# Performance work log

Measured on AMD Instinct MI355X. Metric: run time of the kernel, lower is better.

Reference implementation:

```python
import jax, jax.numpy as jnp
import numpy as np

B, N, E, FIN, H, D = 256, 1024, 8192, 8, 4, 5
HD = H * D            # GATv2: 4 heads * 5 dim, concat -> 20
OBS = N               # flattened obs length
AOUT = 64             # action_space_output_dim (aggregator output)
HID = 256             # hidden_size
NOUT = 64             # num_outputs (logits)
NEG = 0.2             # GATv2 leaky_relu negative slope
EPS = 1e-5            # batchnorm eps


def setup_inputs() -> dict:
    key = jax.random.key(0)
    ks = jax.random.split(key, 16)
    def lin(k, i, o):
        return (jax.random.normal(k, (i, o), jnp.float32) / np.sqrt(i)).astype(jnp.float32)
    return {
        "x": jax.random.normal(ks[0], (B, N, FIN), jnp.float32),
        "obs": jax.random.normal(ks[1], (B, OBS), jnp.float32),
        "edge_index": jax.random.randint(ks[2], (2, E), 0, N),
        # GATv2 layer 0 (in=FIN) and layer 1 (in=HD)
        "Wl0": lin(ks[3], FIN, HD), "Wr0": lin(ks[4], FIN, HD),
        "att0": (jax.random.normal(ks[5], (H, D), jnp.float32) * 0.1), "b0": jnp.zeros((HD,), jnp.float32),
        "Wl1": lin(ks[6], HD, HD), "Wr1": lin(ks[7], HD, HD),
        "att1": (jax.random.normal(ks[8], (H, D), jnp.float32) * 0.1), "b1": jnp.zeros((HD,), jnp.float32),
        # BatchNorm params per layer (over feature dim)
        "g0": jnp.ones((HD,), jnp.float32), "be0": jnp.zeros((HD,), jnp.float32),
        "g1": jnp.ones((HD,), jnp.float32), "be1": jnp.zeros((HD,), jnp.float32),
        # aggregator linear (mean pool -> action-space dim)
        "Wagg": lin(ks[9], HD, AOUT), "bagg": jnp.zeros((AOUT,), jnp.float32),
        # logits MLP: cat(agg, obs) -> HID -> HID//2 -> NOUT (tanh activations)
        "W1": lin(ks[10], AOUT + OBS, HID), "bh1": jnp.zeros((HID,), jnp.float32),
        "W2": lin(ks[11], HID, HID // 2), "bh2": jnp.zeros((HID // 2,), jnp.float32),
        "Wout": lin(ks[12], HID // 2, NOUT), "bout": jnp.zeros((NOUT,), jnp.float32),
    }


def _gatv2_single(x, src, dst, Wl, Wr, att, bias):
    # x: [N, Fin]; src/dst: [Es] (with self loops)
    xl = (x @ Wl).reshape(N, H, D)
    xr = (x @ Wr).reshape(N, H, D)
    m = jax.nn.leaky_relu(xl[src] + xr[dst], NEG)        # [Es, H, D]
    e = jnp.einsum('ehd,hd->eh', m, att)                 # [Es, H]
    emax = jax.ops.segment_max(e, dst, num_segments=N)   # every node has a self loop
    p = jnp.exp(e - emax[dst])
    s = jax.ops.segment_sum(p, dst, num_segments=N)
    alpha = p / s[dst]                                   # softmax over incoming edges
    out = jax.ops.segment_sum(alpha[:, :, None] * xl[src], dst, num_segments=N)
    return out.reshape(N, HD) + bias


def _bn(x, g, b):
    # training-mode batchnorm over all (batch, node) positions, per feature
    mu = x.mean(axis=(0, 1))
    var = x.var(axis=(0, 1))
    return (x - mu) * jax.lax.rsqrt(var + EPS) * g + b


def reference(x, obs, edge_index, Wl0, Wr0, att0, b0, Wl1, Wr1, att1, b1,
              g0, be0, g1, be1, Wagg, bagg, W1, bh1, W2, bh2, Wout, bout):
    loops = jnp.arange(N)
    src = jnp.concatenate([edge_index[0], loops])
    dst = jnp.concatenate([edge_index[1], loops])
    layer = lambda xb, Wl, Wr, att, bias: jax.vmap(
        lambda xn: _gatv2_single(xn, src, dst, Wl, Wr, att, bias))(xb)
    h = layer(x, Wl0, Wr0, att0, b0)       # [B, N, HD]
    h = _bn(h, g0, be0)
    h = layer(h, Wl1, Wr1, att1, b1)
    h = _bn(h, g1, be1)
    agg = h.mean(axis=1) @ Wagg + bagg     # mean graph pooling -> [B, AOUT]
    f = jnp.concatenate([agg, obs], axis=1)
    f = jnp.tanh(f @ W1 + bh1)
    f = jnp.tanh(f @ W2 + bh2)
    return f @ Wout + bout                 # logits [B, NOUT]
```

## Files before the change

### kernel.cpp

```cpp
#include <hip/hip_runtime.h>
#include <hip/hip_bf16.h>
#include <math.h>

typedef unsigned short u16;
typedef __attribute__((ext_vector_type(8))) short short8;
typedef __attribute__((ext_vector_type(4))) float floatx4;

constexpr int kN   = 1024;
constexpr int kB   = 256;
constexpr int kE   = 8192;
constexpr int kHD  = 20;
constexpr float kEps = 1e-5f;

static __device__ __forceinline__ float u16_bf16_to_f32(u16 v) {
  return __uint_as_float(((unsigned)v) << 16);
}
static __device__ __forceinline__ void unpack2(unsigned u, float& a, float& b) {
  a = __uint_as_float(u << 16);
  b = __uint_as_float(u & 0xffff0000u);
}
static __device__ __forceinline__ u16 f2bf(float f) {
  __hip_bfloat16 h = __float2bfloat16(f);
  return *reinterpret_cast<u16*>(&h);
}
static __device__ __forceinline__ unsigned pack_bf16(float a, float b) {
  return (unsigned)f2bf(a) | ((unsigned)f2bf(b) << 16);
}

__global__ __launch_bounds__(64) void detect_kernel(const unsigned* __restrict__ x,
                                                    int* __restrict__ flag) {
  unsigned w = x[threadIdx.x];
  unsigned e = (w >> 7) & 0xFFu;
  bool plaus = (e >= 114u && e <= 136u);
  unsigned long long b = __ballot(plaus);
  if (threadIdx.x == 0) *flag = (__popcll(b) >= 32) ? 1 : 0;
}

struct SmallConv {
  const void* src[17];
  float* dst[17];
  int n[17];
};

__global__ __launch_bounds__(256) void small_conv_kernel(SmallConv a, const int* __restrict__ flag) {
  int t = blockIdx.x;
  int n = a.n[t];
  float* d = a.dst[t];
  if (*flag) {
    const u16* s = (const u16*)a.src[t];
    for (int i = threadIdx.x; i < n; i += 256) d[i] = u16_bf16_to_f32(s[i]);
  } else {
    const float* s = (const float*)a.src[t];
    for (int i = threadIdx.x; i < n; i += 256) d[i] = s[i];
  }
}

__global__ __launch_bounds__(256) void convert_x_kernel(const void* __restrict__ src,
                                                        float* __restrict__ x_f,
                                                        const int* __restrict__ flag) {
  int rid = blockIdx.x * 256 + threadIdx.x;
  int b = rid >> 10, n = rid & 1023;
  float v[8];
  if (*flag) {
    uint4 r = *((const uint4*)((const u16*)src + (size_t)rid * 8));
    unpack2(r.x, v[0], v[1]); unpack2(r.y, v[2], v[3]);
    unpack2(r.z, v[4], v[5]); unpack2(r.w, v[6], v[7]);
  } else {
    const float4* s = (const float4*)((const float*)src + (size_t)rid * 8);
    float4 r0 = s[0], r1 = s[1];
    v[0] = r0.x; v[1] = r0.y; v[2] = r0.z; v[3] = r0.w;
    v[4] = r1.x; v[5] = r1.y; v[6] = r1.z; v[7] = r1.w;
  }
  float* d = x_f + ((size_t)n * kB + b) * 8;
  ((float4*)d)[0] = make_float4(v[0], v[1], v[2], v[3]);
  ((float4*)d)[1] = make_float4(v[4], v[5], v[6], v[7]);
}

static __device__ __forceinline__ void repack_one(const void* src, u16* dst, int c, int N, int srcbf) {
  int n = c % N;
  int t2 = c / N;
  int q = t2 & 3, kb = t2 >> 2;
  int k0 = kb * 32 + q * 8;
  u16 w[8];
  if (srcbf) {
    const u16* s = (const u16*)src;
#pragma unroll
    for (int j = 0; j < 8; j++) w[j] = s[(size_t)(k0 + j) * N + n];
  } else {
    const float* s = (const float*)src;
#pragma unroll
    for (int j = 0; j < 8; j++) w[j] = f2bf(s[(size_t)(k0 + j) * N + n]);
  }
  uint4 out;
  out.x = (unsigned)w[0] | ((unsigned)w[1] << 16);
  out.y = (unsigned)w[2] | ((unsigned)w[3] << 16);
  out.z = (unsigned)w[4] | ((unsigned)w[5] << 16);
  out.w = (unsigned)w[6] | ((unsigned)w[7] << 16);
  *((uint4*)(dst + (size_t)c * 8)) = out;
}

__global__ __launch_bounds__(256) void repack_kernel(const void* __restrict__ W1,
                                                     const void* __restrict__ W2,
                                                     const void* __restrict__ Wout,
                                                     u16* __restrict__ W1p,
                                                     u16* __restrict__ W2p,
                                                     u16* __restrict__ Woutp,
                                                     const int* __restrict__ flag) {
  int c = blockIdx.x * 256 + threadIdx.x;
  int srcbf = *flag;
  if (c < 34816) repack_one(W1, W1p, c, 256, srcbf);
  else if (c < 34816 + 4096) repack_one(W2, W2p, c - 34816, 128, srcbf);
  else if (c < 34816 + 4096 + 1024) repack_one(Wout, Woutp, c - 34816 - 4096, 64, srcbf);
}

__global__ __launch_bounds__(1024) void build_csr_kernel(const int* __restrict__ ei,
                                                         int* __restrict__ csr_off,
                                                         int* __restrict__ csr_src) {
  __shared__ int cnt[kN];
  __shared__ int tmp[kN];
  __shared__ int cur[kN];
  int t = threadIdx.x;
  cnt[t] = 0;
  __syncthreads();
  for (int e = t; e < kE; e += 1024) atomicAdd(&cnt[ei[kE + e]], 1);
  __syncthreads();
  int deg = cnt[t] + 1;
  tmp[t] = deg;
  __syncthreads();
  for (int o = 1; o < kN; o <<= 1) {
    int add = (t >= o) ? tmp[t - o] : 0;
    __syncthreads();
    tmp[t] += add;
    __syncthreads();
  }
  int excl = tmp[t] - deg;
  csr_off[t] = excl;
  cur[t] = excl;
  if (t == kN - 1) csr_off[kN] = tmp[t];
  __syncthreads();
  for (int e = t; e < kE; e += 1024) {
    int s = ei[e], d2 = ei[kE + e];
    int pos = atomicAdd(&cur[d2], 1);
    csr_src[pos] = s;
  }
  int pos = atomicAdd(&cur[t], 1);
  csr_src[pos] = t;
}

__global__ __launch_bounds__(256) void lin0_kernel(const float* __restrict__ x,
                                                   const float* __restrict__ Wl,
                                                   const float* __restrict__ Wr,
                                                   u16* __restrict__ xlb,
                                                   u16* __restrict__ xrb) {
  __shared__ float wl[8 * kHD], wr[8 * kHD];
  int t = threadIdx.x;
  if (t < 8 * kHD) { wl[t] = Wl[t]; wr[t] = Wr[t]; }
  __syncthreads();
  int n = blockIdx.x, b = t;
  const float4* xp = (const float4*)(x + ((size_t)n * kB + b) * 8);
  float xi[8];
  {
    float4 v0 = xp[0], v1 = xp[1];
    xi[0] = v0.x; xi[1] = v0.y; xi[2] = v0.z; xi[3] = v0.w;
    xi[4] = v1.x; xi[5] = v1.y; xi[6] = v1.z; xi[7] = v1.w;
  }
  float ol[kHD], orr[kHD];
#pragma unroll
  for (int f = 0; f < kHD; f++) {
    float al = 0.f, ar = 0.f;
#pragma unroll
    for (int i = 0; i < 8; i++) {
      al = fmaf(xi[i], wl[i * kHD + f], al);
      ar = fmaf(xi[i], wr[i * kHD + f], ar);
    }
    ol[f] = al; orr[f] = ar;
  }
  uint2* pl = (uint2*)(xlb + ((size_t)n * kB + b) * kHD);
  uint2* pr = (uint2*)(xrb + ((size_t)n * kB + b) * kHD);
#pragma unroll
  for (int k = 0; k < 5; k++) {
    pl[k] = make_uint2(pack_bf16(ol[4 * k], ol[4 * k + 1]), pack_bf16(ol[4 * k + 2], ol[4 * k + 3]));
    pr[k] = make_uint2(pack_bf16(orr[4 * k], orr[4 * k + 1]), pack_bf16(orr[4 * k + 2], orr[4 * k + 3]));
  }
}

__global__ __launch_bounds__(256) void lin1_kernel(const u16* __restrict__ hb,
                                                   const float* __restrict__ Wlp,
                                                   const float* __restrict__ Wrp,
                                                   const float* __restrict__ blp,
                                                   const float* __restrict__ brp,
                                                   u16* __restrict__ xlb,
                                                   u16* __restrict__ xrb) {
  __shared__ float wl[kHD * kHD], wr[kHD * kHD], sbl[kHD], sbr[kHD];
  int t = threadIdx.x;
  for (int idx = t; idx < kHD * kHD; idx += 256) { wl[idx] = Wlp[idx]; wr[idx] = Wrp[idx]; }
  if (t < kHD) { sbl[t] = blp[t]; sbr[t] = brp[t]; }
  __syncthreads();
  int n = blockIdx.x, b = t;
  float hv[kHD];
  {
    const uint2* p = (const uint2*)(hb + ((size_t)n * kB + b) * kHD);
#pragma unroll
    for (int k = 0; k < 5; k++) {
      uint2 v = p[k];
      unpack2(v.x, hv[4 * k], hv[4 * k + 1]);
      unpack2(v.y, hv[4 * k + 2], hv[4 * k + 3]);
    }
  }
  float ol[kHD], orr[kHD];
#pragma unroll
  for (int j = 0; j < kHD; j++) {
    float al = sbl[j], ar = sbr[j];
#pragma unroll
    for (int f = 0; f < kHD; f++) {
      al = fmaf(hv[f], wl[f * kHD + j], al);
      ar = fmaf(hv[f], wr[f * kHD + j], ar);
    }
    ol[j] = al; orr[j] = ar;
  }
  uint2* pl = (uint2*)(xlb + ((size_t)n * kB + b) * kHD);
  uint2* pr = (uint2*)(xrb + ((size_t)n * kB + b) * kHD);
#pragma unroll
  for (int k = 0; k < 5; k++) {
    pl[k] = make_uint2(pack_bf16(ol[4 * k], ol[4 * k + 1]), pack_bf16(ol[4 * k + 2], ol[4 * k + 3]));
    pr[k] = make_uint2(pack_bf16(orr[4 * k], orr[4 * k + 1]), pack_bf16(orr[4 * k + 2], orr[4 * k + 3]));
  }
}

__global__ __launch_bounds__(128) void attn_kernel(const u16* __restrict__ xlb,
                                                   const u16* __restrict__ xrb,
                                                   const int* __restrict__ csr_off,
                                                   const int* __restrict__ csr_src,
                                                   const float* __restrict__ att,
                                                   const float* __restrict__ bias,
                                                   u16* __restrict__ hout,
                                                   float* __restrict__ sums) {
  __shared__ float satt[kHD], sbias[kHD];
  __shared__ float red[2][2 * kHD];
  int t = threadIdx.x;
  if (t < kHD) { satt[t] = att[t]; sbias[t] = bias[t]; }
  __syncthreads();
  int n = blockIdx.x >> 1;
  int b = ((blockIdx.x & 1) << 7) | t;

  float xrv[kHD];
  {
    const uint2* p = (const uint2*)(xrb + ((size_t)n * kB + b) * kHD);
#pragma unroll
    for (int k = 0; k < 5; k++) {
      uint2 v = p[k];
      unpack2(v.x, xrv[4 * k], xrv[4 * k + 1]);
      unpack2(v.y, xrv[4 * k + 2], xrv[4 * k + 3]);
    }
  }
  float s[4] = {0.f, 0.f, 0.f, 0.f};
  float acc[kHD];
#pragma unroll
  for (int f = 0; f < kHD; f++) acc[f] = 0.f;

  int beg = csr_off[n], end = csr_off[n + 1];
  uint2 r[5];
  {
    const uint2* p = (const uint2*)(xlb + ((size_t)csr_src[beg] * kB + b) * kHD);
#pragma unroll
    for (int k = 0; k < 5; k++) r[k] = p[k];
  }
  for (int idx = beg; idx < end; idx++) {
    float xs[kHD];
#pragma unroll
    for (int k = 0; k < 5; k++) {
      unpack2(r[k].x, xs[4 * k], xs[4 * k + 1]);
      unpack2(r[k].y, xs[4 * k + 2], xs[4 * k + 3]);
    }
    if (idx + 1 < end) {
      const uint2* p = (const uint2*)(xlb + ((size_t)csr_src[idx + 1] * kB + b) * kHD);
#pragma unroll
      for (int k = 0; k < 5; k++) r[k] = p[k];
    }
#pragma unroll
    for (int hh = 0; hh < 4; hh++) {
      float e = 0.f;
#pragma unroll
      for (int d = 0; d < 5; d++) {
        int f = hh * 5 + d;
        float v = xs[f] + xrv[f];
        v = fmaxf(v, 0.2f * v);
        e = fmaf(v, satt[f], e);
      }
      float p = __expf(e);
      s[hh] += p;
#pragma unroll
      for (int d = 0; d < 5; d++) {
        int f = hh * 5 + d;
        acc[f] = fmaf(p, xs[f], acc[f]);
      }
    }
  }
  float hv[kHD];
#pragma unroll
  for (int hh = 0; hh < 4; hh++) {
    float inv = 1.f / s[hh];
#pragma unroll
    for (int d = 0; d < 5; d++) {
      int f = hh * 5 + d;
      hv[f] = fmaf(acc[f], inv, sbias[f]);
    }
  }
  {
    uint2* ph = (uint2*)(hout + ((size_t)n * kB + b) * kHD);
#pragma unroll
    for (int k = 0; k < 5; k++)
      ph[k] = make_uint2(pack_bf16(hv[4 * k], hv[4 * k + 1]), pack_bf16(hv[4 * k + 2], hv[4 * k + 3]));
  }
  int lane = t & 63, wv = t >> 6;
#pragma unroll
  for (int f = 0; f < kHD; f++) {
    float a = hv[f], q = hv[f] * hv[f];
    for (int o = 32; o > 0; o >>= 1) { a += __shfl_down(a, o); q += __shfl_down(q, o); }
    if (lane == 0) { red[wv][f] = a; red[wv][kHD + f] = q; }
  }
  __syncthreads();
  if (t < 2 * kHD) atomicAdd(&sums[(blockIdx.x & 7) * 2 * kHD + t], red[0][t] + red[1][t]);
}

__global__ __launch_bounds__(256) void fold_kernel(const float* __restrict__ sums,
                                                   const float* __restrict__ g,
                                                   const float* __restrict__ be,
                                                   const float* __restrict__ Wl1,
                                                   const float* __restrict__ Wr1,
                                                   float* __restrict__ Wlp, float* __restrict__ Wrp,
                                                   float* __restrict__ blp, float* __restrict__ brp) {
  __shared__ float a[kHD], c[kHD];
  __shared__ float tot[2 * kHD];
  int t = threadIdx.x;
  if (t < 2 * kHD) {
    float v = 0.f;
    for (int k = 0; k < 8; k++) v += sums[k * 2 * kHD + t];
    tot[t] = v;
  }
  __syncthreads();
  if (t < kHD) {
    const float inv = 1.0f / (float)(kN * kB);
    float mu = tot[t] * inv;
    float var = tot[kHD + t] * inv - mu * mu;
    float av = g[t] * rsqrtf(var + kEps);
    a[t] = av;
    c[t] = be[t] - mu * av;
  }
  __syncthreads();
  for (int idx = t; idx < kHD * kHD; idx += 256) {
    int f = idx / kHD;
    Wlp[idx] = a[f] * Wl1[idx];
    Wrp[idx] = a[f] * Wr1[idx];
  }
  if (t < kHD) {
    float sl = 0.f, sr = 0.f;
    for (int f = 0; f < kHD; f++) {
      sl += c[f] * Wl1[f * kHD + t];
      sr += c[f] * Wr1[f * kHD + t];
    }
    blp[t] = sl;
    brp[t] = sr;
  }
}

__global__ __launch_bounds__(256) void pool_fin_kernel(const u16* __restrict__ hb,
                                                       const float* __restrict__ sums,
                                                       const float* __restrict__ g1,
                                                       const float* __restrict__ be1,
                                                       const float* __restrict__ Wagg,
                                                       const float* __restrict__ bagg,
                                                       const void* __restrict__ obsraw,
                                                       const int* __restrict__ flag,
                                                       u16* __restrict__ finb) {
  int b = blockIdx.x, t = threadIdx.x;
  float acc[kHD];
#pragma unroll
  for (int f = 0; f < kHD; f++) acc[f] = 0.f;
  for (int n = t; n < kN; n += 256) {
    const uint2* p = (const uint2*)(hb + ((size_t)n * kB + b) * kHD);
#pragma unroll
    for (int k = 0; k < 5; k++) {
      uint2 v = p[k];
      float a0, a1, a2, a3;
      unpack2(v.x, a0, a1); unpack2(v.y, a2, a3);
      acc[4 * k] += a0; acc[4 * k + 1] += a1; acc[4 * k + 2] += a2; acc[4 * k + 3] += a3;
    }
  }
  __shared__ float red[4][kHD];
// ... 16 lines not shown
    float var = tot[kHD + t] * inv - mu * mu;
    float a1 = g1[t] * rsqrtf(var + kEps);
    float c1 = be1[t] - mu * a1;
    float pool = (red[0][t] + red[1][t] + red[2][t] + red[3][t]) * (1.0f / kN);
    pv[t] = pool * a1 + c1;
  }
  __syncthreads();
  if (t < 64) {
    float agg = bagg[t];
#pragma unroll
    for (int f = 0; f < kHD; f++) agg = fmaf(pv[f], Wagg[f * 64 + t], agg);
    finb[(size_t)b * 1088 + t] = f2bf(agg);
  }
  if (t < 128) {
    uint4* dst = (uint4*)(finb + (size_t)b * 1088 + 64 + t * 8);
    if (*flag) {
      *dst = *((const uint4*)((const u16*)obsraw + (size_t)b * 1024 + t * 8));
    } else {
      const float4* s = (const float4*)((const float*)obsraw + (size_t)b * 1024 + t * 8);
      float4 r0 = s[0], r1 = s[1];
      uint4 o;
      o.x = pack_bf16(r0.x, r0.y); o.y = pack_bf16(r0.z, r0.w);
      o.z = pack_bf16(r1.x, r1.y); o.w = pack_bf16(r1.z, r1.w);
      *dst = o;
    }
  }
}

__global__ __launch_bounds__(256) void mlp1_kernel(const u16* __restrict__ finb,
                                                   const u16* __restrict__ W1p,
                                                   const float* __restrict__ bh1,
                                                   u16* __restrict__ h1b) {
  int tid = threadIdx.x;
  int wave = tid >> 6, lane = tid & 63;
  int tile = blockIdx.x * 4 + wave;
  int m0 = (tile >> 4) << 4, n0 = (tile & 15) << 4;
  int lo = lane & 15, quad = lane >> 4;
  floatx4 acc = {0.f, 0.f, 0.f, 0.f};
  const u16* ap = finb + (size_t)(m0 + lo) * 1088 + quad * 8;
  const u16* bp = W1p + ((size_t)quad * 256 + n0 + lo) * 8;
  for (int kb = 0; kb < 34; kb++) {
    short8 a = *(const short8*)ap; ap += 32;
    short8 bfr = *(const short8*)bp; bp += 4 * 256 * 8;
    acc = __builtin_amdgcn_mfma_f32_16x16x32_bf16(a, bfr, acc, 0, 0, 0);
  }
  float bias = bh1[n0 + lo];
  u16* op = h1b + (size_t)(m0 + quad * 4) * 256 + n0 + lo;
#pragma unroll
  for (int r = 0; r < 4; r++) op[r * 256] = f2bf(tanhf(acc[r] + bias));
}

__global__ __launch_bounds__(256) void mlp23_kernel(const u16* __restrict__ h1b,
                                                    const u16* __restrict__ W2p,
                                                    const u16* __restrict__ Woutp,
                                                    const float* __restrict__ bh2,
                                                    const float* __restrict__ bout,
                                                    const int* __restrict__ flag,
                                                    void* __restrict__ outv) {
  __shared__ __align__(16) u16 h2s[16][128];
  int tid = threadIdx.x;
  int wave = tid >> 6, lane = tid & 63;
  int lo = lane & 15, quad = lane >> 4;
  int m0 = blockIdx.x * 16;
#pragma unroll
  for (int i = 0; i < 2; i++) {
    int n0 = (wave * 2 + i) * 16;
    floatx4 acc = {0.f, 0.f, 0.f, 0.f};
    const u16* ap = h1b + (size_t)(m0 + lo) * 256 + quad * 8;
    const u16* bp = W2p + ((size_t)quad * 128 + n0 + lo) * 8;
    for (int kb = 0; kb < 8; kb++) {
      short8 a = *(const short8*)ap; ap += 32;
      short8 bfr = *(const short8*)bp; bp += 4 * 128 * 8;
      acc = __builtin_amdgcn_mfma_f32_16x16x32_bf16(a, bfr, acc, 0, 0, 0);
    }
    float bias = bh2[n0 + lo];
#pragma unroll
    for (int r = 0; r < 4; r++) h2s[quad * 4 + r][n0 + lo] = f2bf(tanhf(acc[r] + bias));
  }
  __syncthreads();
  {
    int n0 = wave * 16;
    floatx4 acc = {0.f, 0.f, 0.f, 0.f};
    const u16* bp = Woutp + ((size_t)quad * 64 + n0 + lo) * 8;
    for (int kb = 0; kb < 4; kb++) {
      short8 a = *(const short8*)(&h2s[lo][kb * 32 + quad * 8]);
      short8 bfr = *(const short8*)bp; bp += 4 * 64 * 8;
      acc = __builtin_amdgcn_mfma_f32_16x16x32_bf16(a, bfr, acc, 0, 0, 0);
    }
    float bias = bout[n0 + lo];
    if (*flag) {
      __hip_bfloat16* o = (__hip_bfloat16*)outv;
#pragma unroll
      for (int r = 0; r < 4; r++)
        o[(size_t)(m0 + quad * 4 + r) * 64 + n0 + lo] = __float2bfloat16(acc[r] + bias);
    } else {
      float* o = (float*)outv;
#pragma unroll
      for (int r = 0; r < 4; r++)
        o[(size_t)(m0 + quad * 4 + r) * 64 + n0 + lo] = acc[r] + bias;
    }
  }
}

extern "C" void kernel_launch(void* const* d_in, const int* in_sizes, int n_in,
                              void* d_out, int out_size, void* d_ws, size_t ws_size,
                              hipStream_t stream) {
  const int* ei = (const int*)d_in[2];
  char* ws = (char*)d_ws;

  float* sums0   = (float*)(ws + 0);
  float* sums1   = (float*)(ws + 1280);
  int*   flag    = (int*)(ws + 2560);
  int*   csr_off = (int*)(ws + 2816);
  int*   csr_src = (int*)(ws + 7168);
  float* Wlp     = (float*)(ws + 44288);
  float* Wrp     = (float*)(ws + 45888);
  float* blp     = (float*)(ws + 47488);
  float* brp     = (float*)(ws + 47568);
  float* convf   = (float*)(ws + 47872);
  u16*   W1p     = (u16*)(ws + 60416);
  u16*   W2p     = (u16*)(ws + 617472);
  u16*   Woutp   = (u16*)(ws + 683008);
  u16*   finb    = (u16*)(ws + 699392);
  u16*   h1b     = (u16*)(ws + 1256448);
  float* x_f     = (float*)(ws + 1387520);
  u16*   xlb     = (u16*)(ws + 9776128);
  u16*   xrb     = (u16*)(ws + 20261888);
  u16*   hb      = (u16*)(ws + 30747648);

  const int s_din[17] = {3, 4, 5, 6, 7, 8, 9, 10, 11, 12, 13, 14, 15, 16, 18, 20, 22};
  const int s_n[17]   = {160, 160, 20, 20, 400, 400, 20, 20, 20, 20, 20, 20, 1280, 64, 256, 128, 64};
  SmallConv sc;
  float* fptr[17];
  {
    size_t co = 0;
    for (int i = 0; i < 17; i++) {
      sc.src[i] = d_in[s_din[i]];
      sc.dst[i] = convf + co;
      sc.n[i] = s_n[i];
      fptr[i] = convf + co;
      co += (size_t)s_n[i];
    }
  }
  float* Wl0_f = fptr[0],  *Wr0_f = fptr[1],  *att0_f = fptr[2], *b0_f = fptr[3];
  float* Wl1_f = fptr[4],  *Wr1_f = fptr[5],  *att1_f = fptr[6], *b1_f = fptr[7];
  float* g0_f = fptr[8],   *be0_f = fptr[9],  *g1_f = fptr[10],  *be1_f = fptr[11];
  float* Wagg_f = fptr[12], *bagg_f = fptr[13], *bh1_f = fptr[14], *bh2_f = fptr[15];
  float* bout_f = fptr[16];

  hipMemsetAsync(ws, 0, 2560, stream);
  detect_kernel<<<1, 64, 0, stream>>>((const unsigned*)d_in[0], flag);
  small_conv_kernel<<<17, 256, 0, stream>>>(sc, flag);
  convert_x_kernel<<<1024, 256, 0, stream>>>(d_in[0], x_f, flag);
  repack_kernel<<<156, 256, 0, stream>>>(d_in[17], d_in[19], d_in[21], W1p, W2p, Woutp, flag);
  build_csr_kernel<<<1, 1024, 0, stream>>>(ei, csr_off, csr_src);

  lin0_kernel<<<kN, 256, 0, stream>>>(x_f, Wl0_f, Wr0_f, xlb, xrb);
  attn_kernel<<<2 * kN, 128, 0, stream>>>(xlb, xrb, csr_off, csr_src, att0_f, b0_f, hb, sums0);
  fold_kernel<<<1, 256, 0, stream>>>(sums0, g0_f, be0_f, Wl1_f, Wr1_f, Wlp, Wrp, blp, brp);
  lin1_kernel<<<kN, 256, 0, stream>>>(hb, Wlp, Wrp, blp, brp, xlb, xrb);
  attn_kernel<<<2 * kN, 128, 0, stream>>>(xlb, xrb, csr_off, csr_src, att1_f, b1_f, hb, sums1);
  pool_fin_kernel<<<kB, 256, 0, stream>>>(hb, sums1, g1_f, be1_f, Wagg_f, bagg_f,
                                          d_in[1], flag, finb);
  mlp1_kernel<<<64, 256, 0, stream>>>(finb, W1p, bh1_f, h1b);
  mlp23_kernel<<<16, 256, 0, stream>>>(h1b, W2p, Woutp, bh2_f, bout_f, flag, d_out);
}
```

Baseline: 235.8 us.

## Fuse prep kernels, compute xr inside attention, fold BN in-kernel, merge MLP

Merges detect, small-conversion, x-conversion, weight repack and CSR build into one multi-role prep kernel, and replaces the memset. The attention kernels now compute the right-side projection xr per destination node themselves instead of reading a stored xr buffer, which removes one large write and read per layer. The BatchNorm fold moves into lin1 and attn1. The three MLP kernels become a single kernel that keeps intermediates in shared memory. This cuts launch count and global traffic, but adds redundant per-block fold and projection compute, and leaves the MLP running on only 16 blocks.

After: 239.8 us. Within noise of the previous version (+1.7%).

```diff
diff --git a/kernel.cpp b/kernel.cpp
--- a/kernel.cpp
+++ b/kernel.cpp
@@ -27,13 +27,17 @@
   return (unsigned)f2bf(a) | ((unsigned)f2bf(b) << 16);
 }
 
-__global__ __launch_bounds__(64) void detect_kernel(const unsigned* __restrict__ x,
-                                                    int* __restrict__ flag) {
-  unsigned w = x[threadIdx.x];
-  unsigned e = (w >> 7) & 0xFFu;
-  bool plaus = (e >= 114u && e <= 136u);
-  unsigned long long b = __ballot(plaus);
-  if (threadIdx.x == 0) *flag = (__popcll(b) >= 32) ? 1 : 0;
+static __device__ __forceinline__ int detect_flag(const unsigned* __restrict__ x) {
+  __shared__ int sflag;
+  int t = threadIdx.x;
+  if (t < 64) {
+    unsigned w = x[t];
+    unsigned e = (w >> 7) & 0xFFu;
+    unsigned long long bl = __ballot(e >= 114u && e <= 136u);
+    if (t == 0) sflag = (__popcll(bl) >= 32) ? 1 : 0;
+  }
+  __syncthreads();
+  return sflag;
 }
 
 struct SmallConv {
@@ -42,39 +46,16 @@
   int n[17];
 };
 
-__global__ __launch_bounds__(256) void small_conv_kernel(SmallConv a, const int* __restrict__ flag) {
-  int t = blockIdx.x;
-  int n = a.n[t];
-  float* d = a.dst[t];
-  if (*flag) {
-    const u16* s = (const u16*)a.src[t];
-    for (int i = threadIdx.x; i < n; i += 256) d[i] = u16_bf16_to_f32(s[i]);
-  } else {
-    const float* s = (const float*)a.src[t];
-    for (int i = threadIdx.x; i < n; i += 256) d[i] = s[i];
-  }
-}
-
-__global__ __launch_bounds__(256) void convert_x_kernel(const void* __restrict__ src,
-                                                        float* __restrict__ x_f,
-                                                        const int* __restrict__ flag) {
-  int rid = blockIdx.x * 256 + threadIdx.x;
-  int b = rid >> 10, n = rid & 1023;
-  float v[8];
-  if (*flag) {
-    uint4 r = *((const uint4*)((const u16*)src + (size_t)rid * 8));
-    unpack2(r.x, v[0], v[1]); unpack2(r.y, v[2], v[3]);
-    unpack2(r.z, v[4], v[5]); unpack2(r.w, v[6], v[7]);
-  } else {
-    const float4* s = (const float4*)((const float*)src + (size_t)rid * 8);
-    float4 r0 = s[0], r1 = s[1];
-    v[0] = r0.x; v[1] = r0.y; v[2] = r0.z; v[3] = r0.w;
-    v[4] = r1.x; v[5] = r1.y; v[6] = r1.z; v[7] = r1.w;
-  }
-  float* d = x_f + ((size_t)n * kB + b) * 8;
-  ((float4*)d)[0] = make_float4(v[0], v[1], v[2], v[3]);
-  ((float4*)d)[1] = make_float4(v[4], v[5], v[6], v[7]);
-}
+struct PrepArgs {
+  const unsigned* x;
+  const int* ei;
+  const void* W1; const void* W2; const void* Wout;
+  SmallConv sc;
+  float* x_f;
+  u16* W1p; u16* W2p; u16* Woutp;
+  int* csr_off; int* csr_src;
+  float* sums;
+};
 
 static __device__ __forceinline__ void repack_one(const void* src, u16* dst, int c, int N, int srcbf) {
   int n = c % N;
@@ -99,102 +80,146 @@
   *((uint4*)(dst + (size_t)c * 8)) = out;
 }
 
-__global__ __launch_bounds__(256) void repack_kernel(const void* __restrict__ W1,
-                                                     const void* __restrict__ W2,
-                                                     const void* __restrict__ Wout,
-                                                     u16* __restrict__ W1p,
-                                                     u16* __restrict__ W2p,
-                                                     u16* __restrict__ Woutp,
-                                                     const int* __restrict__ flag) {
-  int c = blockIdx.x * 256 + threadIdx.x;
-  int srcbf = *flag;
-  if (c < 34816) repack_one(W1, W1p, c, 256, srcbf);
-  else if (c < 34816 + 4096) repack_one(W2, W2p, c - 34816, 128, srcbf);
-  else if (c < 34816 + 4096 + 1024) repack_one(Wout, Woutp, c - 34816 - 4096, 64, srcbf);
-}
-
-__global__ __launch_bounds__(1024) void build_csr_kernel(const int* __restrict__ ei,
-                                                         int* __restrict__ csr_off,
-                                                         int* __restrict__ csr_src) {
-  __shared__ int cnt[kN];
-  __shared__ int tmp[kN];
-  __shared__ int cur[kN];
+__global__ __launch_bounds__(256) void prep_kernel(PrepArgs pa) {
+  int bid = blockIdx.x;
   int t = threadIdx.x;
-  cnt[t] = 0;
-  __syncthreads();
-  for (int e = t; e < kE; e += 1024) atomicAdd(&cnt[ei[kE + e]], 1);
-  __syncthreads();
-  int deg = cnt[t] + 1;
-  tmp[t] = deg;
-  __syncthreads();
-  for (int o = 1; o < kN; o <<= 1) {
-    int add = (t >= o) ? tmp[t - o] : 0;
+  if (bid == 0) {
+    __shared__ int cnt[kN];
+    __shared__ int cur[kN];
+    __shared__ int wsum[4];
+    for (int i = t; i < kN; i += 256) cnt[i] = 0;
     __syncthreads();
-    tmp[t] += add;
+    for (int e = t; e < kE; e += 256) atomicAdd(&cnt[pa.ei[kE + e]], 1);
     __syncthreads();
-  }
-  int excl = tmp[t] - deg;
-  csr_off[t] = excl;
-  cur[t] = excl;
-  if (t == kN - 1) csr_off[kN] = tmp[t];
-  __syncthreads();
-  for (int e = t; e < kE; e += 1024) {
-    int s = ei[e], d2 = ei[kE + e];
-    int pos = atomicAdd(&cur[d2], 1);
-    csr_src[pos] = s;
-  }
-  int pos = atomicAdd(&cur[t], 1);
-  csr_src[pos] = t;
-}
-
-__global__ __launch_bounds__(256) void lin0_kernel(const float* __restrict__ x,
+    int d[4], pre[4];
+    int s = 0;
+#pragma unroll
+    for (int j = 0; j < 4; j++) { d[j] = cnt[t * 4 + j] + 1; pre[j] = s; s += d[j]; }
+    int lane = t & 63;
+    int v = s;
+    for (int o = 1; o < 64; o <<= 1) { int u = __shfl_up(v, o); if (lane >= o) v += u; }
+    if (lane == 63) wsum[t >> 6] = v;
+    __syncthreads();
+    int wbase = 0;
+    for (int w = 0; w < (t >> 6); w++) wbase += wsum[w];
+    int base = wbase + v - s;
+#pragma unroll
+    for (int j = 0; j < 4; j++) {
+      pa.csr_off[t * 4 + j] = base + pre[j];
+      cur[t * 4 + j] = base + pre[j];
+    }
+    if (t == 255) pa.csr_off[kN] = wbase + v;
+    __syncthreads();
+    for (int e = t; e < kE; e += 256) {
+      int sv = pa.ei[e], dv = pa.ei[kE + e];
+      int pos = atomicAdd(&cur[dv], 1);
+      pa.csr_src[pos] = sv;
+    }
+    for (int i = t; i < kN; i += 256) {
+      int pos = atomicAdd(&cur[i], 1);
+      pa.csr_src[pos] = i;
+    }
+    return;
+  }
+  int flag = detect_flag(pa.x);
+  if (bid == 1) {
+    for (int i = t; i < 640; i += 256) pa.sums[i] = 0.f;
+    for (int k = 0; k < 17; k++) {
+      int n = pa.sc.n[k];
+      float* d = pa.sc.dst[k];
+      if (flag) {
+        const u16* s = (const u16*)pa.sc.src[k];
+        for (int i = t; i < n; i += 256) d[i] = u16_bf16_to_f32(s[i]);
+      } else {
+        const float* s = (const float*)pa.sc.src[k];
+        for (int i = t; i < n; i += 256) d[i] = s[i];
+      }
+    }
+    return;
+  }
+  if (bid < 158) {
+    int c = (bid - 2) * 256 + t;
+    if (c < 34816) repack_one(pa.W1, pa.W1p, c, 256, flag);
+    else if (c < 34816 + 4096) repack_one(pa.W2, pa.W2p, c - 34816, 128, flag);
+    else if (c < 34816 + 4096 + 1024) repack_one(pa.Wout, pa.Woutp, c - 34816 - 4096, 64, flag);
+    return;
+  }
+  int rid = (bid - 158) * 256 + t;
+  int b = rid >> 10, n = rid & 1023;
+  float v[8];
+  if (flag) {
+    uint4 r = *((const uint4*)((const u16*)pa.x + (size_t)rid * 8));
+    unpack2(r.x, v[0], v[1]); unpack2(r.y, v[2], v[3]);
+    unpack2(r.z, v[4], v[5]); unpack2(r.w, v[6], v[7]);
+  } else {
+    const float4* s = (const float4*)((const float*)pa.x + (size_t)rid * 8);
+    float4 r0 = s[0], r1 = s[1];
+    v[0] = r0.x; v[1] = r0.y; v[2] = r0.z; v[3] = r0.w;
+    v[4] = r1.x; v[5] = r1.y; v[6] = r1.z; v[7] = r1.w;
+  }
+  float* d = pa.x_f + ((size_t)n * kB + b) * 8;
+  ((float4*)d)[0] = make_float4(v[0], v[1], v[2], v[3]);
+  ((float4*)d)[1] = make_float4(v[4], v[5], v[6], v[7]);
+}
+
+__global__ __launch_bounds__(256) void lin0_kernel(const float* __restrict__ x_f,
                                                    const float* __restrict__ Wl,
-                                                   const float* __restrict__ Wr,
-                                                   u16* __restrict__ xlb,
-                                                   u16* __restrict__ xrb) {
-  __shared__ float wl[8 * kHD], wr[8 * kHD];
+                                                   u16* __restrict__ xlb) {
+  __shared__ float wl[160];
   int t = threadIdx.x;
-  if (t < 8 * kHD) { wl[t] = Wl[t]; wr[t] = Wr[t]; }
+  if (t < 160) wl[t] = Wl[t];
   __syncthreads();
   int n = blockIdx.x, b = t;
-  const float4* xp = (const float4*)(x + ((size_t)n * kB + b) * 8);
+  const float4* xp = (const float4*)(x_f + ((size_t)n * kB + b) * 8);
   float xi[8];
   {
     float4 v0 = xp[0], v1 = xp[1];
     xi[0] = v0.x; xi[1] = v0.y; xi[2] = v0.z; xi[3] = v0.w;
     xi[4] = v1.x; xi[5] = v1.y; xi[6] = v1.z; xi[7] = v1.w;
   }
-  float ol[kHD], orr[kHD];
+  float ol[kHD];
 #pragma unroll
   for (int f = 0; f < kHD; f++) {
-    float al = 0.f, ar = 0.f;
-#pragma unroll
-    for (int i = 0; i < 8; i++) {
-      al = fmaf(xi[i], wl[i * kHD + f], al);
-      ar = fmaf(xi[i], wr[i * kHD + f], ar);
-    }
-    ol[f] = al; orr[f] = ar;
+    float al = 0.f;
+#pragma unroll
+    for (int i = 0; i < 8; i++) al = fmaf(xi[i], wl[i * kHD + f], al);
+    ol[f] = al;
   }
   uint2* pl = (uint2*)(xlb + ((size_t)n * kB + b) * kHD);
-  uint2* pr = (uint2*)(xrb + ((size_t)n * kB + b) * kHD);
-#pragma unroll
-  for (int k = 0; k < 5; k++) {
+#pragma unroll
+  for (int k = 0; k < 5; k++)
     pl[k] = make_uint2(pack_bf16(ol[4 * k], ol[4 * k + 1]), pack_bf16(ol[4 * k + 2], ol[4 * k + 3]));
-    pr[k] = make_uint2(pack_bf16(orr[4 * k], orr[4 * k + 1]), pack_bf16(orr[4 * k + 2], orr[4 * k + 3]));
-  }
 }
 
 __global__ __launch_bounds__(256) void lin1_kernel(const u16* __restrict__ hb,
-                                                   const float* __restrict__ Wlp,
-                                                   const float* __restrict__ Wrp,
-                                                   const float* __restrict__ blp,
-                                                   const float* __restrict__ brp,
-                                                   u16* __restrict__ xlb,
-                                                   u16* __restrict__ xrb) {
-  __shared__ float wl[kHD * kHD], wr[kHD * kHD], sbl[kHD], sbr[kHD];
+                                                   const float* __restrict__ sums0,
+                                                   const float* __restrict__ g0,
+                                                   const float* __restrict__ be0,
+                                                   const float* __restrict__ Wl1,
+                                                   u16* __restrict__ xlb) {
+  __shared__ float wl[400], sbl[kHD], afold[kHD], cfold[kHD], tot[2 * kHD];
   int t = threadIdx.x;
-  for (int idx = t; idx < kHD * kHD; idx += 256) { wl[idx] = Wlp[idx]; wr[idx] = Wrp[idx]; }
-  if (t < kHD) { sbl[t] = blp[t]; sbr[t] = brp[t]; }
+  if (t < 2 * kHD) {
+    float v = 0.f;
+    for (int k = 0; k < 8; k++) v += sums0[k * 2 * kHD + t];
+    tot[t] = v;
+  }
+  __syncthreads();
+  if (t < kHD) {
+    const float inv = 1.0f / (float)(kN * kB);
+    float mu = tot[t] * inv;
+    float var = tot[kHD + t] * inv - mu * mu;
+    float a = g0[t] * rsqrtf(var + kEps);
+    afold[t] = a;
+    cfold[t] = be0[t] - mu * a;
+  }
+  __syncthreads();
+  for (int idx = t; idx < 400; idx += 256) wl[idx] = afold[idx / kHD] * Wl1[idx];
+  if (t < kHD) {
+    float s = 0.f;
+    for (int f = 0; f < kHD; f++) s += cfold[f] * Wl1[f * kHD + t];
+    sbl[t] = s;
+  }
   __syncthreads();
   int n = blockIdx.x, b = t;
   float hv[kHD];
@@ -207,50 +232,65 @@
       unpack2(v.y, hv[4 * k + 2], hv[4 * k + 3]);
     }
   }
-  float ol[kHD], orr[kHD];
+  float ol[kHD];
 #pragma unroll
   for (int j = 0; j < kHD; j++) {
-    float al = sbl[j], ar = sbr[j];
-#pragma unroll
-    for (int f = 0; f < kHD; f++) {
-      al = fmaf(hv[f], wl[f * kHD + j], al);
-      ar = fmaf(hv[f], wr[f * kHD + j], ar);
-    }
-    ol[j] = al; orr[j] = ar;
+    float al = sbl[j];
+#pragma unroll
+    for (int f = 0; f < kHD; f++) al = fmaf(hv[f], wl[f * kHD + j], al);
+    ol[j] = al;
   }
   uint2* pl = (uint2*)(xlb + ((size_t)n * kB + b) * kHD);
-  uint2* pr = (uint2*)(xrb + ((size_t)n * kB + b) * kHD);
-#pragma unroll
-  for (int k = 0; k < 5; k++) {
+#pragma unroll
+  for (int k = 0; k < 5; k++)
     pl[k] = make_uint2(pack_bf16(ol[4 * k], ol[4 * k + 1]), pack_bf16(ol[4 * k + 2], ol[4 * k + 3]));
-    pr[k] = make_uint2(pack_bf16(orr[4 * k], orr[4 * k + 1]), pack_bf16(orr[4 * k + 2], orr[4 * k + 3]));
-  }
-}
-
-__global__ __launch_bounds__(128) void attn_kernel(const u16* __restrict__ xlb,
-                                                   const u16* __restrict__ xrb,
-                                                   const int* __restrict__ csr_off,
-                                                   const int* __restrict__ csr_src,
-                                                   const float* __restrict__ att,
-                                                   const float* __restrict__ bias,
-                                                   u16* __restrict__ hout,
-                                                   float* __restrict__ sums) {
-  __shared__ float satt[kHD], sbias[kHD];
+}
+
+static __device__ __forceinline__ void attn_core(const u16* __restrict__ xlb,
+                                                 const int* __restrict__ csr_src,
+                                                 const int* __restrict__ ssrc,
+                                                 int beg, int deg, int b,
+                                                 const float* satt, const float* sbias,
+                                                 float (&red)[2][2 * kHD],
+                                                 int n, int bsw,
+                                                 u16* __restrict__ hout,
+                                                 float* __restrict__ sums) {
+  float xrv[kHD];
+  (void)xrv;
+}
+
+__global__ __launch_bounds__(128) void attn0_kernel(const u16* __restrict__ xlb,
+                                                    const float* __restrict__ x_f,
+                                                    const float* __restrict__ Wr0,
+                                                    const float* __restrict__ att,
+                                                    const float* __restrict__ bias,
+                                                    const int* __restrict__ csr_off,
+                                                    const int* __restrict__ csr_src,
+                                                    u16* __restrict__ hout,
+                                                    float* __restrict__ sums) {
+  __shared__ float satt[kHD], sbias[kHD], swr[160];
   __shared__ float red[2][2 * kHD];
+  __shared__ int ssrc[128];
   int t = threadIdx.x;
   if (t < kHD) { satt[t] = att[t]; sbias[t] = bias[t]; }
-  __syncthreads();
+  for (int i = t; i < 160; i += 128) swr[i] = Wr0[i];
   int n = blockIdx.x >> 1;
+  int beg = csr_off[n], end = csr_off[n + 1];
+  int deg = end - beg;
+  for (int i = t; i < deg && i < 128; i += 128) ssrc[i] = csr_src[beg + i];
+  __syncthreads();
   int b = ((blockIdx.x & 1) << 7) | t;
-
   float xrv[kHD];
   {
-    const uint2* p = (const uint2*)(xrb + ((size_t)n * kB + b) * kHD);
-#pragma unroll
-    for (int k = 0; k < 5; k++) {
-      uint2 v = p[k];
-      unpack2(v.x, xrv[4 * k], xrv[4 * k + 1]);
-      unpack2(v.y, xrv[4 * k + 2], xrv[4 * k + 3]);
+    const float4* xp = (const float4*)(x_f + ((size_t)n * kB + b) * 8);
+    float4 v0 = xp[0], v1 = xp[1];
+    float xi[8] = {v0.x, v0.y, v0.z, v0.w, v1.x, v1.y, v1.z, v1.w};
+#pragma unroll
+    for (int f = 0; f < kHD; f++) {
+      float a = 0.f;
+#pragma unroll
+      for (int i = 0; i < 8; i++) a = fmaf(xi[i], swr[i * kHD + f], a);
+      xrv[f] = a;
     }
   }
   float s[4] = {0.f, 0.f, 0.f, 0.f};
@@ -258,31 +298,25 @@
 #pragma unroll
   for (int f = 0; f < kHD; f++) acc[f] = 0.f;
 
-  int beg = csr_off[n], end = csr_off[n + 1];
-  uint2 r[5];
-  {
-    const uint2* p = (const uint2*)(xlb + ((size_t)csr_src[beg] * kB + b) * kHD);
-#pragma unroll
-    for (int k = 0; k < 5; k++) r[k] = p[k];
-  }
-  for (int idx = beg; idx < end; idx++) {
+  auto loadrow = [&](int i, uint2 (&rr)[5]) {
+    int srcn = (i < 128) ? ssrc[i] : csr_src[beg + i];
+    const uint2* p = (const uint2*)(xlb + ((size_t)srcn * kB + b) * kHD);
+#pragma unroll
+    for (int k = 0; k < 5; k++) rr[k] = p[k];
+  };
+  auto consume = [&](uint2 (&rr)[5]) {
     float xs[kHD];
 #pragma unroll
     for (int k = 0; k < 5; k++) {
-      unpack2(r[k].x, xs[4 * k], xs[4 * k + 1]);
-      unpack2(r[k].y, xs[4 * k + 2], xs[4 * k + 3]);
-    }
-    if (idx + 1 < end) {
-      const uint2* p = (const uint2*)(xlb + ((size_t)csr_src[idx + 1] * kB + b) * kHD);
-#pragma unroll
-      for (int k = 0; k < 5; k++) r[k] = p[k];
+      unpack2(rr[k].x, xs[4 * k], xs[4 * k + 1]);
+      unpack2(rr[k].y, xs[4 * k + 2], xs[4 * k + 3]);
     }
 #pragma unroll
     for (int hh = 0; hh < 4; hh++) {
       float e = 0.f;
 #pragma unroll
-      for (int d = 0; d < 5; d++) {
-        int f = hh * 5 + d;
+      for (int d2 = 0; d2 < 5; d2++) {
+        int f = hh * 5 + d2;
         float v = xs[f] + xrv[f];
         v = fmaxf(v, 0.2f * v);
         e = fmaf(v, satt[f], e);
@@ -290,19 +324,32 @@
       float p = __expf(e);
       s[hh] += p;
 #pragma unroll
-      for (int d = 0; d < 5; d++) {
-        int f = hh * 5 + d;
+      for (int d2 = 0; d2 < 5; d2++) {
+        int f = hh * 5 + d2;
         acc[f] = fmaf(p, xs[f], acc[f]);
       }
     }
-  }
+  };
+
+  uint2 r0[5], r1[5];
+  loadrow(0, r0);
+  if (deg > 1) loadrow(1, r1);
+  int i = 0;
+  for (; i + 1 < deg; i += 2) {
+    consume(r0);
+    if (i + 2 < deg) loadrow(i + 2, r0);
+    consume(r1);
+    if (i + 3 < deg) loadrow(i + 3, r1);
+  }
+  if (i < deg) consume(r0);
+
   float hv[kHD];
 #pragma unroll
   for (int hh = 0; hh < 4; hh++) {
     float inv = 1.f / s[hh];
 #pragma unroll
-    for (int d = 0; d < 5; d++) {
-      int f = hh * 5 + d;
+    for (int d2 = 0; d2 < 5; d2++) {
+      int f = hh * 5 + d2;
       hv[f] = fmaf(acc[f], inv, sbias[f]);
     }
   }
@@ -323,45 +370,145 @@
   if (t < 2 * kHD) atomicAdd(&sums[(blockIdx.x & 7) * 2 * kHD + t], red[0][t] + red[1][t]);
 }
 
-__global__ __launch_bounds__(256) void fold_kernel(const float* __restrict__ sums,
-                                                   const float* __restrict__ g,
-                                                   const float* __restrict__ be,
-                                                   const float* __restrict__ Wl1,
-                                                   const float* __restrict__ Wr1,
-                                                   float* __restrict__ Wlp, float* __restrict__ Wrp,
-                                                   float* __restrict__ blp, float* __restrict__ brp) {
-  __shared__ float a[kHD], c[kHD];
-  __shared__ float tot[2 * kHD];
+__global__ __launch_bounds__(128) void attn1_kernel(const u16* __restrict__ xlb,
+                                                    const u16* __restrict__ hb,
+                                                    const float* __restrict__ sums0,
+                                                    const float* __restrict__ g0,
+                                                    const float* __restrict__ be0,
+                                                    const float* __restrict__ Wr1,
+                                                    const float* __restrict__ att,
+                                                    const float* __restrict__ bias,
+                                                    const int* __restrict__ csr_off,
+                                                    const int* __restrict__ csr_src,
+                                                    u16* __restrict__ hout,
+                                                    float* __restrict__ sums) {
+  __shared__ float satt[kHD], sbias[kHD], swr[400], sbr[kHD];
+  __shared__ float afold[kHD], cfold[kHD], tot[2 * kHD];
+  __shared__ float red[2][2 * kHD];
+  __shared__ int ssrc[128];
   int t = threadIdx.x;
-  if (t < 2 * kHD) {
+  if (t < kHD) { satt[t] = att[t]; sbias[t] = bias[t]; }
+  if (t >= 64 && t < 64 + 2 * kHD) {
+    int j = t - 64;
     float v = 0.f;
-    for (int k = 0; k < 8; k++) v += sums[k * 2 * kHD + t];
-    tot[t] = v;
-  }
+    for (int k = 0; k < 8; k++) v += sums0[k * 2 * kHD + j];
+    tot[j] = v;
+  }
+  int n = blockIdx.x >> 1;
+  int beg = csr_off[n], end = csr_off[n + 1];
+  int deg = end - beg;
+  for (int i = t; i < deg && i < 128; i += 128) ssrc[i] = csr_src[beg + i];
   __syncthreads();
   if (t < kHD) {
     const float inv = 1.0f / (float)(kN * kB);
     float mu = tot[t] * inv;
     float var = tot[kHD + t] * inv - mu * mu;
-    float av = g[t] * rsqrtf(var + kEps);
-    a[t] = av;
-    c[t] = be[t] - mu * av;
-  }
-  __syncthreads();
-  for (int idx = t; idx < kHD * kHD; idx += 256) {
-    int f = idx / kHD;
-    Wlp[idx] = a[f] * Wl1[idx];
-    Wrp[idx] = a[f] * Wr1[idx];
-  }
+    float a = g0[t] * rsqrtf(var + kEps);
+    afold[t] = a;
+    cfold[t] = be0[t] - mu * a;
+  }
+  __syncthreads();
+  for (int idx = t; idx < 400; idx += 128) swr[idx] = afold[idx / kHD] * Wr1[idx];
   if (t < kHD) {
-    float sl = 0.f, sr = 0.f;
-    for (int f = 0; f < kHD; f++) {
-      sl += c[f] * Wl1[f * kHD + t];
-      sr += c[f] * Wr1[f * kHD + t];
-    }
-    blp[t] = sl;
-    brp[t] = sr;
-  }
+    float sv = 0.f;
+    for (int f = 0; f < kHD; f++) sv = fmaf(cfold[f], Wr1[f * kHD + t], sv);
+    sbr[t] = sv;
+  }
+  __syncthreads();
+  int b = ((blockIdx.x & 1) << 7) | t;
+  float xrv[kHD];
+  {
+    float hv0[kHD];
+    const uint2* p = (const uint2*)(hb + ((size_t)n * kB + b) * kHD);
+#pragma unroll
+    for (int k = 0; k < 5; k++) {
+      uint2 v = p[k];
+      unpack2(v.x, hv0[4 * k], hv0[4 * k + 1]);
+      unpack2(v.y, hv0[4 * k + 2], hv0[4 * k + 3]);
+    }
+#pragma unroll
+    for (int j = 0; j < kHD; j++) {
+      float a = sbr[j];
+#pragma unroll
+      for (int f = 0; f < kHD; f++) a = fmaf(hv0[f], swr[f * kHD + j], a);
+      xrv[j] = a;
+    }
+  }
+  float s[4] = {0.f, 0.f, 0.f, 0.f};
+  float acc[kHD];
+#pragma unroll
+  for (int f = 0; f < kHD; f++) acc[f] = 0.f;
+
+  auto loadrow = [&](int i, uint2 (&rr)[5]) {
+    int srcn = (i < 128) ? ssrc[i] : csr_src[beg + i];
+    const uint2* p = (const uint2*)(xlb + ((size_t)srcn * kB + b) * kHD);
+#pragma unroll
+    for (int k = 0; k < 5; k++) rr[k] = p[k];
+  };
+  auto consume = [&](uint2 (&rr)[5]) {
+    float xs[kHD];
+#pragma unroll
+    for (int k = 0; k < 5; k++) {
+      unpack2(rr[k].x, xs[4 * k], xs[4 * k + 1]);
+      unpack2(rr[k].y, xs[4 * k + 2], xs[4 * k + 3]);
+    }
+#pragma unroll
+    for (int hh = 0; hh < 4; hh++) {
+      float e = 0.f;
+#pragma unroll
+      for (int d2 = 0; d2 < 5; d2++) {
+        int f = hh * 5 + d2;
+        float v = xs[f] + xrv[f];
+        v = fmaxf(v, 0.2f * v);
+        e = fmaf(v, satt[f], e);
+      }
+      float p = __expf(e);
+      s[hh] += p;
+#pragma unroll
+      for (int d2 = 0; d2 < 5; d2++) {
+        int f = hh * 5 + d2;
+        acc[f] = fmaf(p, xs[f], acc[f]);
+      }
+    }
+  };
+
+  uint2 r0[5], r1[5];
+  loadrow(0, r0);
+  if (deg > 1) loadrow(1, r1);
+  int i = 0;
+  for (; i + 1 < deg; i += 2) {
+    consume(r0);
+    if (i + 2 < deg) loadrow(i + 2, r0);
+    consume(r1);
+    if (i + 3 < deg) loadrow(i + 3, r1);
+  }
+  if (i < deg) consume(r0);
+
+  float hv[kHD];
+#pragma unroll
+  for (int hh = 0; hh < 4; hh++) {
+    float inv = 1.f / s[hh];
+#pragma unroll
+    for (int d2 = 0; d2 < 5; d2++) {
+      int f = hh * 5 + d2;
+      hv[f] = fmaf(acc[f], inv, sbias[f]);
+    }
+  }
+  {
+    uint2* ph = (uint2*)(hout + ((size_t)n * kB + b) * kHD);
+#pragma unroll
+    for (int k = 0; k < 5; k++)
+      ph[k] = make_uint2(pack_bf16(hv[4 * k], hv[4 * k + 1]), pack_bf16(hv[4 * k + 2], hv[4 * k + 3]));
+  }
+  int lane = t & 63, wv = t >> 6;
+#pragma unroll
+  for (int f = 0; f < kHD; f++) {
+    float a = hv[f], q = hv[f] * hv[f];
+    for (int o = 32; o > 0; o >>= 1) { a += __shfl_down(a, o); q += __shfl_down(q, o); }
+    if (lane == 0) { red[wv][f] = a; red[wv][kHD + f] = q; }
+  }
+  __syncthreads();
+  if (t < 2 * kHD) atomicAdd(&sums[(blockIdx.x & 7) * 2 * kHD + t], red[0][t] + red[1][t]);
 }
 
 __global__ __launch_bounds__(256) void pool_fin_kernel(const u16* __restrict__ hb,
@@ -371,8 +518,9 @@
                                                        const float* __restrict__ Wagg,
                                                        const float* __restrict__ bagg,
                                                        const void* __restrict__ obsraw,
-                                                       const int* __restrict__ flag,
+                                                       const unsigned* __restrict__ xdet,
                                                        u16* __restrict__ finb) {
+  int flag = detect_flag(xdet);
   int b = blockIdx.x, t = threadIdx.x;
   float acc[kHD];
 #pragma unroll
@@ -419,11 +567,11 @@
   }
   if (t < 128) {
     uint4* dst = (uint4*)(finb + (size_t)b * 1088 + 64 + t * 8);
-    if (*flag) {
+    if (flag) {
       *dst = *((const uint4*)((const u16*)obsraw + (size_t)b * 1024 + t * 8));
     } else {
-      const float4* s = (const float4*)((const float*)obsraw + (size_t)b * 1024 + t * 8);
-      float4 r0 = s[0], r1 = s[1];
+      const float4* sp = (const float4*)((const float*)obsraw + (size_t)b * 1024 + t * 8);
+      float4 r0 = sp[0], r1 = sp[1];
       uint4 o;
       o.x = pack_bf16(r0.x, r0.y); o.y = pack_bf16(r0.z, r0.w);
       o.z = pack_bf16(r1.x, r1.y); o.w = pack_bf16(r1.z, r1.w);
@@ -432,68 +580,77 @@
   }
 }
 
-__global__ __launch_bounds__(256) void mlp1_kernel(const u16* __restrict__ finb,
-                                                   const u16* __restrict__ W1p,
-                                                   const float* __restrict__ bh1,
-                                                   u16* __restrict__ h1b) {
-  int tid = threadIdx.x;
-  int wave = tid >> 6, lane = tid & 63;
-  int tile = blockIdx.x * 4 + wave;
-  int m0 = (tile >> 4) << 4, n0 = (tile & 15) << 4;
-  int lo = lane & 15, quad = lane >> 4;
-  floatx4 acc = {0.f, 0.f, 0.f, 0.f};
-  const u16* ap = finb + (size_t)(m0 + lo) * 1088 + quad * 8;
-  const u16* bp = W1p + ((size_t)quad * 256 + n0 + lo) * 8;
-  for (int kb = 0; kb < 34; kb++) {
-    short8 a = *(const short8*)ap; ap += 32;
-    short8 bfr = *(const short8*)bp; bp += 4 * 256 * 8;
-    acc = __builtin_amdgcn_mfma_f32_16x16x32_bf16(a, bfr, acc, 0, 0, 0);
-  }
-  float bias = bh1[n0 + lo];
-  u16* op = h1b + (size_t)(m0 + quad * 4) * 256 + n0 + lo;
-#pragma unroll
-  for (int r = 0; r < 4; r++) op[r * 256] = f2bf(tanhf(acc[r] + bias));
-}
-
-__global__ __launch_bounds__(256) void mlp23_kernel(const u16* __restrict__ h1b,
-                                                    const u16* __restrict__ W2p,
-                                                    const u16* __restrict__ Woutp,
-                                                    const float* __restrict__ bh2,
-                                                    const float* __restrict__ bout,
-                                                    const int* __restrict__ flag,
-                                                    void* __restrict__ outv) {
-  __shared__ __align__(16) u16 h2s[16][128];
-  int tid = threadIdx.x;
-  int wave = tid >> 6, lane = tid & 63;
-  int lo = lane & 15, quad = lane >> 4;
+__global__ __launch_bounds__(256) void mlp_kernel(const u16* __restrict__ finb,
+                                                  const u16* __restrict__ W1p,
+                                                  const u16* __restrict__ W2p,
+                                                  const u16* __restrict__ Woutp,
+                                                  const float* __restrict__ bh1,
+                                                  const float* __restrict__ bh2,
+                                                  const float* __restrict__ bout,
+                                                  const unsigned* __restrict__ xdet,
+                                                  void* __restrict__ outv) {
+  __shared__ __align__(16) u16 fins[16][1096];
+  __shared__ __align__(16) u16 h1s[16][264];
+  __shared__ __align__(16) u16 h2s[16][136];
+  int flag = detect_flag(xdet);
+  int t = threadIdx.x;
   int m0 = blockIdx.x * 16;
-#pragma unroll
-  for (int i = 0; i < 2; i++) {
-    int n0 = (wave * 2 + i) * 16;
-    floatx4 acc = {0.f, 0.f, 0.f, 0.f};
-    const u16* ap = h1b + (size_t)(m0 + lo) * 256 + quad * 8;
-    const u16* bp = W2p + ((size_t)quad * 128 + n0 + lo) * 8;
+  for (int r = 0; r < 16; r++) {
+    for (int k = t * 8; k < 1088; k += 2048)
+      *(uint4*)&fins[r][k] = *(const uint4*)(finb + (size_t)(m0 + r) * 1088 + k);
+  }
+  __syncthreads();
+  int wave = t >> 6, lane = t & 63, lo = lane & 15, quad = lane >> 4;
+  {
+    floatx4 acc[4] = {{0.f, 0.f, 0.f, 0.f}, {0.f, 0.f, 0.f, 0.f}, {0.f, 0.f, 0.f, 0.f}, {0.f, 0.f, 0.f, 0.f}};
+    for (int kb = 0; kb < 34; kb++) {
+      short8 a = *(const short8*)&fins[lo][kb * 32 + quad * 8];
+#pragma unroll
+      for (int nt = 0; nt < 4; nt++) {
+        int n0 = (wave * 4 + nt) * 16;
+        short8 bf = *(const short8*)(W1p + ((size_t)(kb * 4 + quad) * 256 + n0 + lo) * 8);
+        acc[nt] = __builtin_amdgcn_mfma_f32_16x16x32_bf16(a, bf, acc[nt], 0, 0, 0);
+      }
+    }
+#pragma unroll
+    for (int nt = 0; nt < 4; nt++) {
+      int n0 = (wave * 4 + nt) * 16;
+      float bias = bh1[n0 + lo];
+#pragma unroll
+      for (int r = 0; r < 4; r++) h1s[quad * 4 + r][n0 + lo] = f2bf(tanhf(acc[nt][r] + bias));
+    }
+  }
+  __syncthreads();
+  {
+    floatx4 acc[2] = {{0.f, 0.f, 0.f, 0.f}, {0.f, 0.f, 0.f, 0.f}};
     for (int kb = 0; kb < 8; kb++) {
-      short8 a = *(const short8*)ap; ap += 32;
-      short8 bfr = *(const short8*)bp; bp += 4 * 128 * 8;
-      acc = __builtin_amdgcn_mfma_f32_16x16x32_bf16(a, bfr, acc, 0, 0, 0);
-    }
-    float bias = bh2[n0 + lo];
-#pragma unroll
-    for (int r = 0; r < 4; r++) h2s[quad * 4 + r][n0 + lo] = f2bf(tanhf(acc[r] + bias));
+      short8 a = *(const short8*)&h1s[lo][kb * 32 + quad * 8];
+#pragma unroll
+      for (int nt = 0; nt < 2; nt++) {
+        int n0 = (wave * 2 + nt) * 16;
+        short8 bf = *(const short8*)(W2p + ((size_t)(kb * 4 + quad) * 128 + n0 + lo) * 8);
+        acc[nt] = __builtin_amdgcn_mfma_f32_16x16x32_bf16(a, bf, acc[nt], 0, 0, 0);
+      }
+    }
+#pragma unroll
+    for (int nt = 0; nt < 2; nt++) {
+      int n0 = (wave * 2 + nt) * 16;
+      float bias = bh2[n0 + lo];
+#pragma unroll
+      for (int r = 0; r < 4; r++) h2s[quad * 4 + r][n0 + lo] = f2bf(tanhf(acc[nt][r] + bias));
+    }
   }
   __syncthreads();
   {
     int n0 = wave * 16;
     floatx4 acc = {0.f, 0.f, 0.f, 0.f};
-    const u16* bp = Woutp + ((size_t)quad * 64 + n0 + lo) * 8;
     for (int kb = 0; kb < 4; kb++) {
-      short8 a = *(const short8*)(&h2s[lo][kb * 32 + quad * 8]);
-      short8 bfr = *(const short8*)bp; bp += 4 * 64 * 8;
-      acc = __builtin_amdgcn_mfma_f32_16x16x32_bf16(a, bfr, acc, 0, 0, 0);
+      short8 a = *(const short8*)&h2s[lo][kb * 32 + quad * 8];
+      short8 bf = *(const short8*)(Woutp + ((size_t)(kb * 4 + quad) * 64 + n0 + lo) * 8);
+      acc = __builtin_amdgcn_mfma_f32_16x16x32_bf16(a, bf, acc, 0, 0, 0);
     }
     float bias = bout[n0 + lo];
-    if (*flag) {
+    if (flag) {
       __hip_bfloat16* o = (__hip_bfloat16*)outv;
 #pragma unroll
       for (int r = 0; r < 4; r++)
@@ -515,23 +672,17 @@
 
   float* sums0   = (float*)(ws + 0);
   float* sums1   = (float*)(ws + 1280);
-  int*   flag    = (int*)(ws + 2560);
   int*   csr_off = (int*)(ws + 2816);
   int*   csr_src = (int*)(ws + 7168);
-  float* Wlp     = (float*)(ws + 44288);
-  float* Wrp     = (float*)(ws + 45888);
-  float* blp     = (float*)(ws + 47488);
-  float* brp     = (float*)(ws + 47568);
-  float* convf   = (float*)(ws + 47872);
-  u16*   W1p     = (u16*)(ws + 60416);
-  u16*   W2p     = (u16*)(ws + 617472);
-  u16*   Woutp   = (u16*)(ws + 683008);
-  u16*   finb    = (u16*)(ws + 699392);
-  u16*   h1b     = (u16*)(ws + 1256448);
-  float* x_f     = (float*)(ws + 1387520);
-  u16*   xlb     = (u16*)(ws + 9776128);
-  u16*   xrb     = (u16*)(ws + 20261888);
-  u16*   hb      = (u16*)(ws + 30747648);
+  float* convf   = (float*)(ws + 44288);
+  u16*   W1p     = (u16*)(ws + 56832);
+  u16*   W2p     = (u16*)(ws + 613888);
+  u16*   Woutp   = (u16*)(ws + 679424);
+  u16*   finb    = (u16*)(ws + 695808);
+  float* x_f     = (float*)(ws + 1253120);
+  u16*   xlb     = (u16*)(ws + 9641728);
+  u16*   hb      = (u16*)(ws + 20127488);
+  u16*   hb2     = (u16*)(ws + 30613248);
 
   const int s_din[17] = {3, 4, 5, 6, 7, 8, 9, 10, 11, 12, 13, 14, 15, 16, 18, 20, 22};
   const int s_n[17]   = {160, 160, 20, 20, 400, 400, 20, 20, 20, 20, 20, 20, 1280, 64, 256, 128, 64};
@@ -553,20 +704,24 @@
   float* Wagg_f = fptr[12], *bagg_f = fptr[13], *bh1_f = fptr[14], *bh2_f = fptr[15];
   float* bout_f = fptr[16];
 
-  hipMemsetAsync(ws, 0, 2560, stream);
-  detect_kernel<<<1, 64, 0, stream>>>((const unsigned*)d_in[0], flag);
-  small_conv_kernel<<<17, 256, 0, stream>>>(sc, flag);
-  convert_x_kernel<<<1024, 256, 0, stream>>>(d_in[0], x_f, flag);
-  repack_kernel<<<156, 256, 0, stream>>>(d_in[17], d_in[19], d_in[21], W1p, W2p, Woutp, flag);
-  build_csr_kernel<<<1, 1024, 0, stream>>>(ei, csr_off, csr_src);
-
-  lin0_kernel<<<kN, 256, 0, stream>>>(x_f, Wl0_f, Wr0_f, xlb, xrb);
-  attn_kernel<<<2 * kN, 128, 0, stream>>>(xlb, xrb, csr_off, csr_src, att0_f, b0_f, hb, sums0);
-  fold_kernel<<<1, 256, 0, stream>>>(sums0, g0_f, be0_f, Wl1_f, Wr1_f, Wlp, Wrp, blp, brp);
-  lin1_kernel<<<kN, 256, 0, stream>>>(hb, Wlp, Wrp, blp, brp, xlb, xrb);
-  attn_kernel<<<2 * kN, 128, 0, stream>>>(xlb, xrb, csr_off, csr_src, att1_f, b1_f, hb, sums1);
-  pool_fin_kernel<<<kB, 256, 0, stream>>>(hb, sums1, g1_f, be1_f, Wagg_f, bagg_f,
-                                          d_in[1], flag, finb);
-  mlp1_kernel<<<64, 256, 0, stream>>>(finb, W1p, bh1_f, h1b);
-  mlp23_kernel<<<16, 256, 0, stream>>>(h1b, W2p, Woutp, bh2_f, bout_f, flag, d_out);
-}
+  PrepArgs pa;
+  pa.x = (const unsigned*)d_in[0];
+  pa.ei = ei;
+  pa.W1 = d_in[17]; pa.W2 = d_in[19]; pa.Wout = d_in[21];
+  pa.sc = sc;
+  pa.x_f = x_f;
+  pa.W1p = W1p; pa.W2p = W2p; pa.Woutp = Woutp;
+  pa.csr_off = csr_off; pa.csr_src = csr_src;
+  pa.sums = sums0;
+
+  prep_kernel<<<1182, 256, 0, stream>>>(pa);
+  lin0_kernel<<<kN, 256, 0, stream>>>(x_f, Wl0_f, xlb);
+  attn0_kernel<<<2 * kN, 128, 0, stream>>>(xlb, x_f, Wr0_f, att0_f, b0_f, csr_off, csr_src, hb, sums0);
+  lin1_kernel<<<kN, 256, 0, stream>>>(hb, sums0, g0_f, be0_f, Wl1_f, xlb);
+  attn1_kernel<<<2 * kN, 128, 0, stream>>>(xlb, hb, sums0, g0_f, be0_f, Wr1_f, att1_f, b1_f,
+                                           csr_off, csr_src, hb2, sums1);
+  pool_fin_kernel<<<kB, 256, 0, stream>>>(hb2, sums1, g1_f, be1_f, Wagg_f, bagg_f,
+                                          d_in[1], (const unsigned*)d_in[0], finb);
+  mlp_kernel<<<16, 256, 0, stream>>>(finb, W1p, W2p, Woutp, bh1_f, bh2_f, bout_f,
+                                     (const unsigned*)d_in[0], d_out);
+}
```
